# Kernel tuning notes

Measured on AMD Instinct MI355X. Metric: run time of the kernel, lower is better.

## Reference

```python
import jax, jax.numpy as jnp
import numpy as np

E = 500_000
N = 30_000
R = 6
H = 256
OE = 256
OUT = 1
L = 3          # num_layers
A = 2          # num_aux + 1 branches


def setup_inputs() -> dict:
    key = jax.random.key(0)
    ks = jax.random.split(key, 9)
    x = jax.random.normal(ks[0], (E, H), dtype=jnp.float32)
    rbf = jax.random.normal(ks[1], (E, R), dtype=jnp.float32)
    i = jax.random.randint(ks[2], (E,), 0, N, dtype=jnp.int64)
    # parameters (stored in [in, out] convention)
    s = 1.0 / np.sqrt(H)
    W_rbf = jax.random.normal(ks[3], (R, H), dtype=jnp.float32) / np.sqrt(R)
    W_up = jax.random.normal(ks[4], (A, H, OE), dtype=jnp.float32) * s
    W_hidden = jax.random.normal(ks[5], (A, L, OE, OE), dtype=jnp.float32) / np.sqrt(OE)
    b_hidden = jnp.zeros((A, L, OE), dtype=jnp.float32)
    W_out = jax.random.normal(ks[6], (A, OE, OUT), dtype=jnp.float32) / np.sqrt(OE)
    return {"x": x, "rbf": rbf, "i": i, "num_nodes": N,
            "W_rbf": W_rbf, "W_up": W_up, "W_hidden": W_hidden,
            "b_hidden": b_hidden, "W_out": W_out}


def reference(x, rbf, i, num_nodes, W_rbf, W_up, W_hidden, b_hidden, W_out):
    # elementwise multiply of per-edge features by radial basis projection,
    # then segment-sum over edge target index -> per-node features [N, H]
    msg = (rbf @ W_rbf) * x                     # [E, H]
    h = jax.ops.segment_sum(msg, i, num_segments=num_nodes)  # [N, H]
    outs = []
    for a in range(A):
        y = h @ W_up[a]                          # [N, OE]
        for l in range(L):
            y = jax.nn.silu(y @ W_hidden[a, l] + b_hidden[a, l])
        outs.append(y @ W_out[a])               # [N, OUT]
    return tuple(outs)
```

## Files before the change

### kernel.cpp

```cpp
#include <hip/hip_runtime.h>

#define E_EDGES 500000
#define N_NODES 30000
#define H_DIM   256

typedef float  floatx4 __attribute__((ext_vector_type(4)));
typedef short  shortx4 __attribute__((ext_vector_type(4)));
typedef short  shortx8 __attribute__((ext_vector_type(8)));
typedef __bf16 bf16x8  __attribute__((ext_vector_type(8)));

__device__ inline short f2bf(float f) {
    unsigned u = __builtin_bit_cast(unsigned, f);
    u += 0x7fffu + ((u >> 16) & 1u);
    return (short)(u >> 16);
}
__device__ inline float bf2f(short s) {
    unsigned u = ((unsigned)(unsigned short)s) << 16;
    return __builtin_bit_cast(float, u);
}

__global__ __launch_bounds__(256) void prep_weights(
    const float* __restrict__ wup, const float* __restrict__ whid,
    short* __restrict__ wfrag)
{
    int g   = blockIdx.x * 256 + threadIdx.x;
    int mat = g >> 13;
    int grp = g & 8191;
    int a = mat >> 2, lay = mat & 3;
    const float* src = (lay == 0) ? (wup + a * 65536)
                                  : (whid + (a * 3 + lay - 1) * 65536);
    int ks  = grp >> 10;
    int rem = grp & 1023;
    int ntg = rem >> 6;
    int lane = rem & 63;
    int q = lane >> 4, c = lane & 15;
    int col = ntg * 16 + c;
    int k0  = ks * 32 + q * 8;
    shortx8 v;
#pragma unroll
    for (int j = 0; j < 8; j++) v[j] = f2bf(src[(k0 + j) * 256 + col]);
    ((shortx8*)wfrag)[g] = v;
}

__global__ __launch_bounds__(256) void hist_kernel(
    const int* __restrict__ idx, int* __restrict__ counts)
{
    int e = blockIdx.x * 256 + threadIdx.x;
    if (e < E_EDGES) atomicAdd(&counts[idx[e]], 1);
}

__global__ __launch_bounds__(1024) void scan_kernel(
    const int* __restrict__ counts, int* __restrict__ offsets,
    int* __restrict__ cursor)
{
    const int t = threadIdx.x;
    const int lane = t & 63, wave = t >> 6;
    const int base = t * 30;
    int local[30];
    int s = 0;
#pragma unroll
    for (int j = 0; j < 30; j++) {
        int c = (base + j < N_NODES) ? counts[base + j] : 0;
        local[j] = s;
        s += c;
    }
    int incl = s;
#pragma unroll
    for (int d = 1; d < 64; d <<= 1) {
        int v = __shfl_up(incl, d);
        if (lane >= d) incl += v;
    }
    __shared__ int part[16];
    if (lane == 63) part[wave] = incl;
    __syncthreads();
    if (t == 0) {
        int run = 0;
#pragma unroll
        for (int k = 0; k < 16; k++) { int v = part[k]; part[k] = run; run += v; }
    }
    __syncthreads();
    int excl = part[wave] + incl - s;
#pragma unroll
    for (int j = 0; j < 30; j++) {
        int n = base + j;
        if (n < N_NODES) { offsets[n] = excl + local[j]; cursor[n] = excl + local[j]; }
    }
    if (t == 1023) offsets[N_NODES] = excl + s;
}

__global__ __launch_bounds__(256) void scatter_ids(
    const int* __restrict__ idx, int* __restrict__ cursor,
    int* __restrict__ edge_list)
{
    int e = blockIdx.x * 256 + threadIdx.x;
    if (e >= E_EDGES) return;
    int pos = atomicAdd(&cursor[idx[e]], 1);
    edge_list[pos] = e;
}

__global__ __launch_bounds__(256) void gather_nodes(
    const float* __restrict__ x, const float* __restrict__ rbf,
    const int* __restrict__ edge_list, const int* __restrict__ offsets,
    const float* __restrict__ wrbf, float* __restrict__ h)
{
    int node = blockIdx.x * 4 + (threadIdx.x >> 6);
    if (node >= N_NODES) return;
    int lane = threadIdx.x & 63;

    const floatx4* wr4 = (const floatx4*)wrbf;
    floatx4 wr[6];
#pragma unroll
    for (int k = 0; k < 6; k++) wr[k] = wr4[k * 64 + lane];

    int beg = offsets[node], end = offsets[node + 1];
    floatx4 acc = {0.f, 0.f, 0.f, 0.f};
    for (int j = beg; j < end; j++) {
        int e = edge_list[j];
        float r0 = rbf[e * 6 + 0], r1 = rbf[e * 6 + 1], r2 = rbf[e * 6 + 2];
        float r3 = rbf[e * 6 + 3], r4 = rbf[e * 6 + 4], r5 = rbf[e * 6 + 5];
        floatx4 xv = ((const floatx4*)x)[(size_t)e * 64 + lane];
        floatx4 p = r0 * wr[0] + r1 * wr[1] + r2 * wr[2]
                  + r3 * wr[3] + r4 * wr[4] + r5 * wr[5];
        acc += p * xv;
    }
    ((floatx4*)h)[(size_t)node * 64 + lane] = acc;
}

__global__ __launch_bounds__(256, 2) void mlp_kernel(
    const float* __restrict__ h, const short* __restrict__ wfrag,
    const float* __restrict__ bias, const float* __restrict__ wout,
    float* __restrict__ out)
{
    __shared__ __align__(16) short ylds[2][64 * 264];
    const int t = threadIdx.x;
    const int wave = t >> 6, lane = t & 63, q = lane >> 4, c15 = lane & 15;
    const int n0 = blockIdx.x * 64;
    const floatx4 fzero = {0.f, 0.f, 0.f, 0.f};

    for (int a = 0; a < 2; a++) {
#pragma unroll
        for (int j = 0; j < 16; j++) {
            int f = t + j * 256;
            int r = f >> 6, c4 = f & 63;
            floatx4 v = fzero;
            if (n0 + r < N_NODES) v = ((const floatx4*)h)[(size_t)(n0 + r) * 64 + c4];
            shortx4 s4 = { f2bf(v.x), f2bf(v.y), f2bf(v.z), f2bf(v.w) };
            *(shortx4*)&ylds[0][r * 264 + c4 * 4] = s4;
        }
        __syncthreads();

        int src = 0;
        for (int lay = 0; lay < 4; lay++) {
            const bf16x8* wf = (const bf16x8*)(wfrag + (size_t)(a * 4 + lay) * 65536);
            floatx4 acc[4][4];
#pragma unroll
            for (int mt = 0; mt < 4; mt++)
#pragma unroll
                for (int nt = 0; nt < 4; nt++) acc[mt][nt] = fzero;

#pragma unroll
            for (int ks = 0; ks < 8; ks++) {
                bf16x8 afr[4], bfr[4];
#pragma unroll
                for (int mt = 0; mt < 4; mt++)
                    afr[mt] = *(const bf16x8*)&ylds[src][(mt * 16 + c15) * 264 + ks * 32 + q * 8];
#pragma unroll
                for (int nt = 0; nt < 4; nt++)
                    bfr[nt] = wf[(ks * 16 + wave * 4 + nt) * 64 + lane];
#pragma unroll
                for (int mt = 0; mt < 4; mt++)
#pragma unroll
                    for (int nt = 0; nt < 4; nt++)
                        acc[mt][nt] = __builtin_amdgcn_mfma_f32_16x16x32_bf16(
                            afr[mt], bfr[nt], acc[mt][nt], 0, 0, 0);
            }

            int dst = 1 - src;
            float bv[4];
#pragma unroll
            for (int nt = 0; nt < 4; nt++)
                bv[nt] = (lay >= 1) ? bias[(a * 3 + lay - 1) * 256 + wave * 64 + nt * 16 + c15]
                                    : 0.0f;
#pragma unroll
            for (int mt = 0; mt < 4; mt++) {
#pragma unroll
                for (int nt = 0; nt < 4; nt++) {
#pragma unroll
                    for (int rg = 0; rg < 4; rg++) {
                        float v = acc[mt][nt][rg] + bv[nt];
                        if (lay >= 1) v = v / (1.0f + __expf(-v));
                        int row = mt * 16 + q * 4 + rg;
                        int col = wave * 64 + nt * 16 + c15;
                        ylds[dst][row * 264 + col] = f2bf(v);
                    }
                }
            }
            __syncthreads();
            src = dst;
        }

        {
            int r  = wave * 16 + (lane >> 2);
            int cq = lane & 3;
            float s = 0.0f;
#pragma unroll 16
            for (int c = cq * 64; c < cq * 64 + 64; c++)
                s += bf2f(ylds[src][r * 264 + c]) * wout[a * 256 + c];
            s += __shfl_xor(s, 1);
            s += __shfl_xor(s, 2);
            if (cq == 0 && n0 + r < N_NODES) out[a * N_NODES + n0 + r] = s;
        }
        __syncthreads();
    }
}

extern "C" void kernel_launch(void* const* d_in, const int* in_sizes, int n_in,
                              void* d_out, int out_size, void* d_ws, size_t ws_size,
                              hipStream_t stream)
{
    const float* x    = (const float*)d_in[0];
    const float* rbf  = (const float*)d_in[1];
    const int*   idx  = (const int*)d_in[2];
    const float* wrbf = (const float*)d_in[4];
    const float* wup  = (const float*)d_in[5];
    const float* whid = (const float*)d_in[6];
    const float* bias = (const float*)d_in[7];
    const float* wout = (const float*)d_in[8];
    float* out = (float*)d_out;

    char* ws = (char*)d_ws;
    float* h         = (float*)ws;                                   ws += (size_t)N_NODES * H_DIM * sizeof(float);
    short* wfrag     = (short*)ws;                                   ws += (size_t)8 * 65536 * sizeof(short);
    int*   counts    = (int*)ws;                                     ws += (size_t)N_NODES * sizeof(int);
    int*   offsets   = (int*)ws;                                     ws += (size_t)(N_NODES + 1) * sizeof(int);
    int*   cursor    = (int*)ws;                                     ws += (size_t)N_NODES * sizeof(int);
    int*   edge_list = (int*)ws;

    hipMemsetAsync(counts, 0, (size_t)N_NODES * sizeof(int), stream);
    prep_weights<<<256, 256, 0, stream>>>(wup, whid, wfrag);
    hist_kernel<<<(E_EDGES + 255) / 256, 256, 0, stream>>>(idx, counts);
    scan_kernel<<<1, 1024, 0, stream>>>(counts, offsets, cursor);
    scatter_ids<<<(E_EDGES + 255) / 256, 256, 0, stream>>>(idx, cursor, edge_list);
    gather_nodes<<<(N_NODES + 3) / 4, 256, 0, stream>>>(x, rbf, edge_list, offsets, wrbf, h);
    mlp_kernel<<<(N_NODES + 63) / 64, 256, 0, stream>>>(h, wfrag, bias, wout, out);
}
```

Before: 876.5 us.

## Single-buffer MLP LDS for higher occupancy, prefetch edge ids, vectorize loads

```diff
diff --git a/kernel.cpp b/kernel.cpp
--- a/kernel.cpp
+++ b/kernel.cpp
@@ -114,24 +114,29 @@
 
     int beg = offsets[node], end = offsets[node + 1];
     floatx4 acc = {0.f, 0.f, 0.f, 0.f};
-    for (int j = beg; j < end; j++) {
-        int e = edge_list[j];
-        float r0 = rbf[e * 6 + 0], r1 = rbf[e * 6 + 1], r2 = rbf[e * 6 + 2];
-        float r3 = rbf[e * 6 + 3], r4 = rbf[e * 6 + 4], r5 = rbf[e * 6 + 5];
-        floatx4 xv = ((const floatx4*)x)[(size_t)e * 64 + lane];
-        floatx4 p = r0 * wr[0] + r1 * wr[1] + r2 * wr[2]
-                  + r3 * wr[3] + r4 * wr[4] + r5 * wr[5];
-        acc += p * xv;
+    if (beg < end) {
+        int e = edge_list[beg];
+        for (int j = beg; j < end; j++) {
+            int e_next = (j + 1 < end) ? edge_list[j + 1] : e;
+            floatx4 xv = __builtin_nontemporal_load(
+                             (const floatx4*)x + (size_t)e * 64 + lane);
+            float r0 = rbf[e * 6 + 0], r1 = rbf[e * 6 + 1], r2 = rbf[e * 6 + 2];
+            float r3 = rbf[e * 6 + 3], r4 = rbf[e * 6 + 4], r5 = rbf[e * 6 + 5];
+            floatx4 p = r0 * wr[0] + r1 * wr[1] + r2 * wr[2]
+                      + r3 * wr[3] + r4 * wr[4] + r5 * wr[5];
+            acc += p * xv;
+            e = e_next;
+        }
     }
     ((floatx4*)h)[(size_t)node * 64 + lane] = acc;
 }
 
-__global__ __launch_bounds__(256, 2) void mlp_kernel(
+__global__ __launch_bounds__(256, 4) void mlp_kernel(
     const float* __restrict__ h, const short* __restrict__ wfrag,
     const float* __restrict__ bias, const float* __restrict__ wout,
     float* __restrict__ out)
 {
-    __shared__ __align__(16) short ylds[2][64 * 264];
+    __shared__ __align__(16) short ylds[64 * 264];
     const int t = threadIdx.x;
     const int wave = t >> 6, lane = t & 63, q = lane >> 4, c15 = lane & 15;
     const int n0 = blockIdx.x * 64;
@@ -139,17 +144,20 @@
 
     for (int a = 0; a < 2; a++) {
 #pragma unroll
-        for (int j = 0; j < 16; j++) {
+        for (int j = 0; j < 8; j++) {
             int f = t + j * 256;
-            int r = f >> 6, c4 = f & 63;
-            floatx4 v = fzero;
-            if (n0 + r < N_NODES) v = ((const floatx4*)h)[(size_t)(n0 + r) * 64 + c4];
-            shortx4 s4 = { f2bf(v.x), f2bf(v.y), f2bf(v.z), f2bf(v.w) };
-            *(shortx4*)&ylds[0][r * 264 + c4 * 4] = s4;
+            int r = f >> 5, c8 = f & 31;
+            floatx4 v0 = fzero, v1 = fzero;
+            if (n0 + r < N_NODES) {
+                v0 = ((const floatx4*)h)[(size_t)(n0 + r) * 64 + c8 * 2];
+                v1 = ((const floatx4*)h)[(size_t)(n0 + r) * 64 + c8 * 2 + 1];
+            }
+            shortx8 s8 = { f2bf(v0.x), f2bf(v0.y), f2bf(v0.z), f2bf(v0.w),
+                           f2bf(v1.x), f2bf(v1.y), f2bf(v1.z), f2bf(v1.w) };
+            *(shortx8*)&ylds[r * 264 + c8 * 8] = s8;
         }
         __syncthreads();
 
-        int src = 0;
         for (int lay = 0; lay < 4; lay++) {
             const bf16x8* wf = (const bf16x8*)(wfrag + (size_t)(a * 4 + lay) * 65536);
             floatx4 acc[4][4];
@@ -160,22 +168,21 @@
 
 #pragma unroll
             for (int ks = 0; ks < 8; ks++) {
-                bf16x8 afr[4], bfr[4];
-#pragma unroll
-                for (int mt = 0; mt < 4; mt++)
-                    afr[mt] = *(const bf16x8*)&ylds[src][(mt * 16 + c15) * 264 + ks * 32 + q * 8];
+                bf16x8 bfr[4];
 #pragma unroll
                 for (int nt = 0; nt < 4; nt++)
                     bfr[nt] = wf[(ks * 16 + wave * 4 + nt) * 64 + lane];
 #pragma unroll
-                for (int mt = 0; mt < 4; mt++)
+                for (int mt = 0; mt < 4; mt++) {
+                    bf16x8 afr = *(const bf16x8*)&ylds[(mt * 16 + c15) * 264 + ks * 32 + q * 8];
 #pragma unroll
                     for (int nt = 0; nt < 4; nt++)
                         acc[mt][nt] = __builtin_amdgcn_mfma_f32_16x16x32_bf16(
-                            afr[mt], bfr[nt], acc[mt][nt], 0, 0, 0);
-            }
-
-            int dst = 1 - src;
+                            afr, bfr[nt], acc[mt][nt], 0, 0, 0);
+                }
+            }
+            __syncthreads();
+
             float bv[4];
 #pragma unroll
             for (int nt = 0; nt < 4; nt++)
@@ -191,21 +198,28 @@
                         if (lay >= 1) v = v / (1.0f + __expf(-v));
                         int row = mt * 16 + q * 4 + rg;
                         int col = wave * 64 + nt * 16 + c15;
-                        ylds[dst][row * 264 + col] = f2bf(v);
+                        ylds[row * 264 + col] = f2bf(v);
                     }
                 }
             }
             __syncthreads();
-            src = dst;
         }
 
         {
             int r  = wave * 16 + (lane >> 2);
             int cq = lane & 3;
+            const floatx4* w4 = (const floatx4*)(wout + a * 256);
             float s = 0.0f;
-#pragma unroll 16
-            for (int c = cq * 64; c < cq * 64 + 64; c++)
-                s += bf2f(ylds[src][r * 264 + c]) * wout[a * 256 + c];
+#pragma unroll
+            for (int b8 = 0; b8 < 8; b8++) {
+                shortx8 yv = *(const shortx8*)&ylds[r * 264 + cq * 64 + b8 * 8];
+                floatx4 w0 = w4[cq * 16 + b8 * 2];
+                floatx4 w1 = w4[cq * 16 + b8 * 2 + 1];
+                s += bf2f(yv[0]) * w0.x + bf2f(yv[1]) * w0.y
+                   + bf2f(yv[2]) * w0.z + bf2f(yv[3]) * w0.w
+                   + bf2f(yv[4]) * w1.x + bf2f(yv[5]) * w1.y
+                   + bf2f(yv[6]) * w1.z + bf2f(yv[7]) * w1.w;
+            }
             s += __shfl_xor(s, 1);
             s += __shfl_xor(s, 2);
             if (cq == 0 && n0 + r < N_NODES) out[a * N_NODES + n0 + r] = s;
@@ -229,11 +243,11 @@
     float* out = (float*)d_out;
 
     char* ws = (char*)d_ws;
-    float* h         = (float*)ws;                                   ws += (size_t)N_NODES * H_DIM * sizeof(float);
-    short* wfrag     = (short*)ws;                                   ws += (size_t)8 * 65536 * sizeof(short);
-    int*   counts    = (int*)ws;                                     ws += (size_t)N_NODES * sizeof(int);
-    int*   offsets   = (int*)ws;                                     ws += (size_t)(N_NODES + 1) * sizeof(int);
-    int*   cursor    = (int*)ws;                                     ws += (size_t)N_NODES * sizeof(int);
+    float* h         = (float*)ws;     ws += (size_t)N_NODES * H_DIM * sizeof(float);
+    short* wfrag     = (short*)ws;     ws += (size_t)8 * 65536 * sizeof(short);
+    int*   counts    = (int*)ws;       ws += (size_t)N_NODES * sizeof(int);
+    int*   offsets   = (int*)ws;       ws += (size_t)(N_NODES + 1) * sizeof(int);
+    int*   cursor    = (int*)ws;       ws += (size_t)N_NODES * sizeof(int);
     int*   edge_list = (int*)ws;
 
     hipMemsetAsync(counts, 0, (size_t)N_NODES * sizeof(int), stream);
```

Result: slower. 897.3 us (+2.4%).
